# Performance work log

Measured on AMD Instinct MI355X. Metric: run time of the kernel, lower is better.

Reference implementation:

```python
import jax, jax.numpy as jnp
import numpy as np

MAX_BITS = 8   # codes are stored at 8 bits (max of supported_bits), 4 codes per int32
W_BITS = 4     # active bit-width -> lut has 2**W_BITS entries per output row


def setup_inputs() -> dict:
    key = jax.random.key(0)
    k1, k2, k3 = jax.random.split(key, 3)
    B, S = 1, 2048
    OUT, IN = 8192, 8192
    x = jax.random.normal(k1, (B, S, IN), dtype=jnp.float32)
    qweight = jax.random.randint(k2, (OUT, IN // 4), 0, 2147483647, dtype=jnp.int32)
    # per-output-channel lookup table for w_bits=4 -> 16 entries
    lut = jax.random.normal(k3, (OUT, 2 ** W_BITS), dtype=jnp.float32)
    return {"x": x, "qweight": qweight, "lut": lut}


def dequant_kbit(qweight, lut, w_bits):
    # qweight: (O, K//4) int32 -> 8-bit codes (O, K)
    O = qweight.shape[0]
    shifts = jnp.array([0, 8, 16, 24], dtype=jnp.int32)
    codes = (qweight[:, :, None] >> shifts) & 0xFF          # (O, K//4, 4)
    codes = codes.reshape(O, -1)                             # (O, K)
    # any-precision: top w_bits of the 8-bit code index the w_bits LUT
    idx = codes >> (MAX_BITS - w_bits)                       # (O, K) in [0, 2**w_bits)
    weight = jnp.take_along_axis(lut, idx, axis=1)           # (O, K)
    return weight


def reference(x, qweight, lut):
    # bulk path of AnyprecisionLinear.forward (tokens > 8): dequant then matmul
    weight = dequant_kbit(qweight, lut, W_BITS)              # (O, K)
    out = jnp.einsum('bsk,ok->bso', x, weight)               # (B, S, O)
    return out
```

## Files before the change

kernel.cpp:

```cpp
#include <hip/hip_runtime.h>
#include <stdint.h>


#define M_DIM 2048
#define N_DIM 8192
#define K_DIM 8192
#define BM 128
#define BN 128
#define BK 64

typedef __bf16 bf16x8 __attribute__((ext_vector_type(8)));
typedef float f32x16 __attribute__((ext_vector_type(16)));

__device__ __forceinline__ unsigned int f2bf(float f) {
  unsigned int u = __float_as_uint(f);
  return (u + 0x7FFFu + ((u >> 16) & 1u)) >> 16;
}

__global__ __launch_bounds__(256) void dequant_kernel(
    const int4* __restrict__ qw4,
    const float* __restrict__ lut,
    unsigned short* __restrict__ wb) {
  __shared__ unsigned int slut[4 * 16 * 64];
  const int wave = threadIdx.x >> 6;
  const int lane = threadIdx.x & 63;
  const int row = (blockIdx.x << 2) + wave;

  unsigned int* tbl = slut + wave * (16 * 64) + lane;
  const float* lr = lut + row * 16;
#pragma unroll
  for (int e = 0; e < 16; ++e) tbl[e * 64] = f2bf(lr[e]);

  const int4* src = qw4 + (size_t)row * 512 + lane;
  unsigned short* dst = wb + (size_t)row * K_DIM + lane * 16;

#pragma unroll
  for (int it = 0; it < 8; ++it) {
    int4 q = src[it * 64];
    unsigned int w[4] = {(unsigned int)q.x, (unsigned int)q.y,
                         (unsigned int)q.z, (unsigned int)q.w};
    unsigned int v[16];
#pragma unroll
    for (int j = 0; j < 4; ++j) {
#pragma unroll
      for (int k = 0; k < 4; ++k)
        v[j * 4 + k] = tbl[((w[j] >> (8 * k + 4)) & 15u) * 64];
    }
    uint4 o0, o1;
    o0.x = v[0] | (v[1] << 16);   o0.y = v[2]  | (v[3] << 16);
    o0.z = v[4] | (v[5] << 16);   o0.w = v[6]  | (v[7] << 16);
    o1.x = v[8] | (v[9] << 16);   o1.y = v[10] | (v[11] << 16);
    o1.z = v[12] | (v[13] << 16); o1.w = v[14] | (v[15] << 16);
    uint4* dp = (uint4*)(dst + it * 1024);
    dp[0] = o0;
    dp[1] = o1;
  }
}

__global__ __launch_bounds__(256) void cvt_x_kernel(
    const float4* __restrict__ x4, unsigned int* __restrict__ xb) {
  const int idx = blockIdx.x * 256 + threadIdx.x;
  float4 a = x4[2 * idx];
  float4 b = x4[2 * idx + 1];
  uint4 o;
  o.x = f2bf(a.x) | (f2bf(a.y) << 16);
  o.y = f2bf(a.z) | (f2bf(a.w) << 16);
  o.z = f2bf(b.x) | (f2bf(b.y) << 16);
  o.w = f2bf(b.z) | (f2bf(b.w) << 16);
  ((uint4*)xb)[idx] = o;
}

__global__ __launch_bounds__(256) void gemm_bt(
    const unsigned short* __restrict__ A,
    const unsigned short* __restrict__ B,
    float* __restrict__ C) {
  __shared__ __align__(16) unsigned short sA[BM * BK];
  __shared__ __align__(16) unsigned short sB[BN * BK];

  const int tid = threadIdx.x;
  const int wave = tid >> 6;
  const int lane = tid & 63;
  const int m0 = blockIdx.y * BM;
  const int n0 = blockIdx.x * BN;
  const int wm = (wave & 1) * 64;
  const int wn = (wave >> 1) * 64;

  const int srow = lane >> 3;
  const int scol = ((lane & 7) ^ (lane >> 3)) * 8;

  const int laneN = lane & 31;
  const int half = lane >> 5;
  const int sw = laneN & 7;

  f32x16 acc[2][2];
#pragma unroll
  for (int i = 0; i < 2; ++i)
#pragma unroll
    for (int j = 0; j < 2; ++j)
#pragma unroll
      for (int r = 0; r < 16; ++r) acc[i][j][r] = 0.0f;

  for (int k0 = 0; k0 < K_DIM; k0 += BK) {
#pragma unroll
    for (int r = 0; r < 4; ++r) {
      const int chunk = wave * 4 + r;
      const int row = chunk * 8 + srow;
      const unsigned short* ga = A + (size_t)(m0 + row) * K_DIM + k0 + scol;
      __builtin_amdgcn_global_load_lds(
          (const __attribute__((address_space(1))) void*)ga,
          (__attribute__((address_space(3))) void*)(sA + chunk * 512),
          16, 0, 0);
      const unsigned short* gb = B + (size_t)(n0 + row) * K_DIM + k0 + scol;
      __builtin_amdgcn_global_load_lds(
          (const __attribute__((address_space(1))) void*)gb,
          (__attribute__((address_space(3))) void*)(sB + chunk * 512),
          16, 0, 0);
    }
    __syncthreads();

#pragma unroll
    for (int kk = 0; kk < BK; kk += 16) {
      const int c = ((kk >> 3) + half) ^ sw;
      bf16x8 af[2], bfr[2];
#pragma unroll
      for (int t = 0; t < 2; ++t) {
        af[t]  = *(const bf16x8*)(sA + (wm + t * 32 + laneN) * BK + c * 8);
        bfr[t] = *(const bf16x8*)(sB + (wn + t * 32 + laneN) * BK + c * 8);
      }
#pragma unroll
      for (int i = 0; i < 2; ++i)
#pragma unroll
        for (int j = 0; j < 2; ++j)
          acc[i][j] = __builtin_amdgcn_mfma_f32_32x32x16_bf16(
              af[i], bfr[j], acc[i][j], 0, 0, 0);
    }
    __syncthreads();
  }

#pragma unroll
  for (int i = 0; i < 2; ++i)
#pragma unroll
    for (int j = 0; j < 2; ++j) {
      const int rbase = m0 + wm + i * 32 + 4 * half;
      const int col = n0 + wn + j * 32 + laneN;
#pragma unroll
      for (int r = 0; r < 16; ++r) {
        const int rrow = rbase + (r & 3) + 8 * (r >> 2);
        C[(size_t)rrow * N_DIM + col] = acc[i][j][r];
      }
    }
}

__global__ void naive_kernel(const float* __restrict__ x,
                             const int* __restrict__ qw,
                             const float* __restrict__ lut,
                             float* __restrict__ out) {
  int o = blockIdx.x * blockDim.x + threadIdx.x;
  int s = blockIdx.y;
  const float* xr = x + (size_t)s * K_DIM;
  const unsigned int* qr = (const unsigned int*)qw + (size_t)o * (K_DIM / 4);
  const float* l = lut + o * 16;
  float acc = 0.f;
  for (int w = 0; w < K_DIM / 4; ++w) {
    unsigned int q = qr[w];
    acc += xr[w * 4 + 0] * l[(q >> 4) & 15u]
         + xr[w * 4 + 1] * l[(q >> 12) & 15u]
         + xr[w * 4 + 2] * l[(q >> 20) & 15u]
         + xr[w * 4 + 3] * l[(q >> 28) & 15u];
  }
  out[(size_t)s * N_DIM + o] = acc;
}

extern "C" void kernel_launch(void* const* d_in, const int* in_sizes, int n_in,
                              void* d_out, int out_size, void* d_ws, size_t ws_size,
                              hipStream_t stream) {
  const float* x   = (const float*)d_in[0];
  const int*   qw  = (const int*)d_in[1];
  const float* lut = (const float*)d_in[2];
  float* out = (float*)d_out;

  const size_t wb_elems = (size_t)N_DIM * K_DIM;
  const size_t xb_elems = (size_t)M_DIM * K_DIM;
  const size_t need = (wb_elems + xb_elems) * sizeof(unsigned short);

  if (ws_size >= need) {
    unsigned short* wb = (unsigned short*)d_ws;
    unsigned short* xb = wb + wb_elems;

    hipLaunchKernelGGL(dequant_kernel, dim3(N_DIM / 4), dim3(256), 0, stream,
                       (const int4*)qw, lut, wb);

    const int n_thr = M_DIM * K_DIM / 8;
    hipLaunchKernelGGL(cvt_x_kernel, dim3(n_thr / 256), dim3(256), 0, stream,
                       (const float4*)x, (unsigned int*)xb);

    dim3 grid(N_DIM / BN, M_DIM / BM);
    hipLaunchKernelGGL(gemm_bt, grid, dim3(256), 0, stream, xb, wb, out);
  } else {
    dim3 grid(N_DIM / 256, M_DIM);
    hipLaunchKernelGGL(naive_kernel, grid, dim3(256), 0, stream, x, qw, lut, out);
  }
}
```

Measured before the change: 501.3 us.

## Rewrite GEMM as 256x256 tile with double-buffered LDS and interleaved prefetch

```diff
diff --git a/kernel.cpp b/kernel.cpp
--- a/kernel.cpp
+++ b/kernel.cpp
@@ -5,12 +5,13 @@
 #define M_DIM 2048
 #define N_DIM 8192
 #define K_DIM 8192
-#define BM 128
-#define BN 128
+#define BM 256
+#define BN 256
 #define BK 64
+#define KT (K_DIM / BK)
 
 typedef __bf16 bf16x8 __attribute__((ext_vector_type(8)));
-typedef float f32x16 __attribute__((ext_vector_type(16)));
+typedef float f32x4 __attribute__((ext_vector_type(4)));
 
 __device__ __forceinline__ unsigned int f2bf(float f) {
   unsigned int u = __float_as_uint(f);
@@ -70,85 +71,177 @@
   ((uint4*)xb)[idx] = o;
 }
 
-__global__ __launch_bounds__(256) void gemm_bt(
+
+__device__ __forceinline__ void stage_q(const unsigned short* __restrict__ g,
+                                        unsigned short* lds_tile, int grow0,
+                                        int qrow, int koff, int wave, int srow,
+                                        int scol) {
+  const unsigned short* src =
+      g + (size_t)(grow0 + qrow + (wave << 3) + srow) * K_DIM + koff + scol;
+  __builtin_amdgcn_global_load_lds(
+      (const __attribute__((address_space(1))) void*)src,
+      (__attribute__((address_space(3))) void*)(lds_tile +
+                                                (qrow + (wave << 3)) * BK),
+      16, 0, 0);
+}
+
+__device__ __forceinline__ void load_a4(const unsigned short* __restrict__ s,
+                                        int row0, int rrow, int rk,
+                                        bf16x8 out[4][2]) {
+#pragma unroll
+  for (int mi = 0; mi < 4; ++mi) {
+    const int row = row0 + mi * 16 + rrow;
+    const int sw = row & 7;
+#pragma unroll
+    for (int ks = 0; ks < 2; ++ks) {
+      const int slot = (ks * 4 + rk) ^ sw;
+      out[mi][ks] = *(const bf16x8*)(s + row * BK + slot * 8);
+    }
+  }
+}
+
+__device__ __forceinline__ void load_b2(const unsigned short* __restrict__ s,
+                                        int row0, int rrow, int rk,
+                                        bf16x8 out[2][2]) {
+#pragma unroll
+  for (int nj = 0; nj < 2; ++nj) {
+    const int row = row0 + nj * 16 + rrow;
+    const int sw = row & 7;
+#pragma unroll
+    for (int ks = 0; ks < 2; ++ks) {
+      const int slot = (ks * 4 + rk) ^ sw;
+      out[nj][ks] = *(const bf16x8*)(s + row * BK + slot * 8);
+    }
+  }
+}
+
+#define MFMA_Q(AH, BH)                                                        \
+  _Pragma("unroll")                                                           \
+  for (int ks = 0; ks < 2; ++ks)                                              \
+    _Pragma("unroll")                                                         \
+    for (int mi = 0; mi < 4; ++mi)                                            \
+      _Pragma("unroll")                                                       \
+      for (int nj = 0; nj < 2; ++nj)                                          \
+        acc[(AH)*4 + mi][(BH)*2 + nj] =                                       \
+            __builtin_amdgcn_mfma_f32_16x16x32_bf16(                          \
+                af[mi][ks], bq[nj][ks], acc[(AH)*4 + mi][(BH)*2 + nj], 0, 0, 0);
+
+#define SBAR asm volatile("s_barrier" ::: "memory")
+
+#define KTILE(T, BF)                                                          \
+  {                                                                           \
+    const int ko1 = (((T) + 1) & (KT - 1)) * BK;                              \
+    const int ko2 = (((T) + 2) & (KT - 1)) * BK;                              \
+    const unsigned short* sa_ = sA[BF];                                       \
+    const unsigned short* sb_ = sB[BF];                                       \
+    unsigned short* naA = sA[(BF) ^ 1];                                       \
+    unsigned short* naB = sB[(BF) ^ 1];                                       \
+    unsigned short* caA = sA[BF];                                             \
+                                                          \
+    load_a4(sa_, wm + 0, rrow, rk, af);                                       \
+    load_b2(sb_, wn + 0, rrow, rk, bq);                                       \
+    stage_q(A, naA, m0, 64, ko1, wave, srow, scol);                           \
+    stage_q(B, naB, n0, 0, ko1, wave, srow, scol);                            \
+    SBAR;                                                                     \
+    __builtin_amdgcn_s_setprio(1);                                            \
+    MFMA_Q(0, 0);                                                             \
+    __builtin_amdgcn_s_setprio(0);                                            \
+    SBAR;                                                                     \
+                                               \
+    load_b2(sb_, wn + 32, rrow, rk, bq);                                      \
+    stage_q(A, naA, m0, 192, ko1, wave, srow, scol);                          \
+    stage_q(B, naB, n0, 64, ko1, wave, srow, scol);                           \
+    SBAR;                                                                     \
+    __builtin_amdgcn_s_setprio(1);                                            \
+    MFMA_Q(0, 1);                                                             \
+    __builtin_amdgcn_s_setprio(0);                                            \
+    SBAR;                                                                     \
+                                               \
+    load_a4(sa_, wm + 64, rrow, rk, af);                                      \
+    stage_q(B, naB, n0, 128, ko1, wave, srow, scol);                          \
+    stage_q(B, naB, n0, 192, ko1, wave, srow, scol);                          \
+    SBAR;                                                                     \
+    __builtin_amdgcn_s_setprio(1);                                            \
+    MFMA_Q(1, 1);                                                             \
+    __builtin_amdgcn_s_setprio(0);                                            \
+    SBAR;                                                                     \
+                                               \
+    load_b2(sb_, wn + 0, rrow, rk, bq);                                       \
+    stage_q(A, caA, m0, 0, ko2, wave, srow, scol);                            \
+    stage_q(A, caA, m0, 128, ko2, wave, srow, scol);                          \
+    SBAR;                                                                     \
+    __builtin_amdgcn_s_setprio(1);                                            \
+    MFMA_Q(1, 0);                                                             \
+    __builtin_amdgcn_s_setprio(0);                                            \
+    asm volatile("s_waitcnt vmcnt(2)" ::: "memory");                          \
+    SBAR;                                                                     \
+  }
+
+__global__ __launch_bounds__(512, 2) void gemm_bt(
     const unsigned short* __restrict__ A,
     const unsigned short* __restrict__ B,
     float* __restrict__ C) {
-  __shared__ __align__(16) unsigned short sA[BM * BK];
-  __shared__ __align__(16) unsigned short sB[BN * BK];
+  __shared__ __align__(16) unsigned short sA[2][BM * BK];
+  __shared__ __align__(16) unsigned short sB[2][BN * BK];
 
   const int tid = threadIdx.x;
   const int wave = tid >> 6;
   const int lane = tid & 63;
-  const int m0 = blockIdx.y * BM;
-  const int n0 = blockIdx.x * BN;
-  const int wm = (wave & 1) * 64;
-  const int wn = (wave >> 1) * 64;
+
+  const int bid = blockIdx.x;
+  const int swz = (bid & 7) * 32 + (bid >> 3);
+  const int m0 = (swz >> 5) * BM;
+  const int n0 = (swz & 31) * BN;
+
+  const int wm = (wave >> 2) * 128;
+  const int wn = (wave & 3) * 64;
 
   const int srow = lane >> 3;
-  const int scol = ((lane & 7) ^ (lane >> 3)) * 8;
-
-  const int laneN = lane & 31;
-  const int half = lane >> 5;
-  const int sw = laneN & 7;
-
-  f32x16 acc[2][2];
-#pragma unroll
-  for (int i = 0; i < 2; ++i)
-#pragma unroll
-    for (int j = 0; j < 2; ++j)
-#pragma unroll
-      for (int r = 0; r < 16; ++r) acc[i][j][r] = 0.0f;
-
-  for (int k0 = 0; k0 < K_DIM; k0 += BK) {
-#pragma unroll
-    for (int r = 0; r < 4; ++r) {
-      const int chunk = wave * 4 + r;
-      const int row = chunk * 8 + srow;
-      const unsigned short* ga = A + (size_t)(m0 + row) * K_DIM + k0 + scol;
-      __builtin_amdgcn_global_load_lds(
-          (const __attribute__((address_space(1))) void*)ga,
-          (__attribute__((address_space(3))) void*)(sA + chunk * 512),
-          16, 0, 0);
-      const unsigned short* gb = B + (size_t)(n0 + row) * K_DIM + k0 + scol;
-      __builtin_amdgcn_global_load_lds(
-          (const __attribute__((address_space(1))) void*)gb,
-          (__attribute__((address_space(3))) void*)(sB + chunk * 512),
-          16, 0, 0);
-    }
-    __syncthreads();
-
-#pragma unroll
-    for (int kk = 0; kk < BK; kk += 16) {
-      const int c = ((kk >> 3) + half) ^ sw;
-      bf16x8 af[2], bfr[2];
-#pragma unroll
-      for (int t = 0; t < 2; ++t) {
-        af[t]  = *(const bf16x8*)(sA + (wm + t * 32 + laneN) * BK + c * 8);
-        bfr[t] = *(const bf16x8*)(sB + (wn + t * 32 + laneN) * BK + c * 8);
-      }
-#pragma unroll
-      for (int i = 0; i < 2; ++i)
-#pragma unroll
-        for (int j = 0; j < 2; ++j)
-          acc[i][j] = __builtin_amdgcn_mfma_f32_32x32x16_bf16(
-              af[i], bfr[j], acc[i][j], 0, 0, 0);
-    }
-    __syncthreads();
-  }
-
-#pragma unroll
-  for (int i = 0; i < 2; ++i)
-#pragma unroll
-    for (int j = 0; j < 2; ++j) {
-      const int rbase = m0 + wm + i * 32 + 4 * half;
-      const int col = n0 + wn + j * 32 + laneN;
-#pragma unroll
-      for (int r = 0; r < 16; ++r) {
-        const int rrow = rbase + (r & 3) + 8 * (r >> 2);
-        C[(size_t)rrow * N_DIM + col] = acc[i][j][r];
-      }
-    }
+  const int scol = ((lane & 7) ^ srow) * 8;
+
+  const int rrow = lane & 15;
+  const int rk = lane >> 4;
+
+  bf16x8 af[4][2];
+  bf16x8 bq[2][2];
+  f32x4 acc[8][4];
+#pragma unroll
+  for (int m = 0; m < 8; ++m)
+#pragma unroll
+    for (int n = 0; n < 4; ++n)
+#pragma unroll
+      for (int r = 0; r < 4; ++r) acc[m][n][r] = 0.0f;
+
+  stage_q(A, sA[0], m0, 0, 0, wave, srow, scol);
+  stage_q(A, sA[0], m0, 64, 0, wave, srow, scol);
+  stage_q(A, sA[0], m0, 128, 0, wave, srow, scol);
+  stage_q(A, sA[0], m0, 192, 0, wave, srow, scol);
+  stage_q(B, sB[0], n0, 0, 0, wave, srow, scol);
+  stage_q(B, sB[0], n0, 64, 0, wave, srow, scol);
+  stage_q(B, sB[0], n0, 128, 0, wave, srow, scol);
+  stage_q(B, sB[0], n0, 192, 0, wave, srow, scol);
+  stage_q(A, sA[1], m0, 0, BK, wave, srow, scol);
+  stage_q(A, sA[1], m0, 128, BK, wave, srow, scol);
+  asm volatile("s_waitcnt vmcnt(2)" ::: "memory");
+  SBAR;
+
+#pragma unroll 1
+  for (int tt = 0; tt < KT / 2; ++tt) {
+    KTILE(2 * tt, 0)
+    KTILE(2 * tt + 1, 1)
+  }
+  asm volatile("s_waitcnt vmcnt(0)" ::: "memory");
+
+  const int crow0 = m0 + wm + 4 * rk;
+  const int ccol0 = n0 + wn + rrow;
+#pragma unroll
+  for (int m = 0; m < 8; ++m)
+#pragma unroll
+    for (int n = 0; n < 4; ++n)
+#pragma unroll
+      for (int r = 0; r < 4; ++r)
+        C[(size_t)(crow0 + m * 16 + r) * N_DIM + ccol0 + n * 16] =
+            acc[m][n][r];
 }
 
 __global__ void naive_kernel(const float* __restrict__ x,
@@ -172,10 +265,10 @@
 }
 
 extern "C" void kernel_launch(void* const* d_in, const int* in_sizes, int n_in,
-                              void* d_out, int out_size, void* d_ws, size_t ws_size,
-                              hipStream_t stream) {
-  const float* x   = (const float*)d_in[0];
-  const int*   qw  = (const int*)d_in[1];
+                              void* d_out, int out_size, void* d_ws,
+                              size_t ws_size, hipStream_t stream) {
+  const float* x = (const float*)d_in[0];
+  const int* qw = (const int*)d_in[1];
   const float* lut = (const float*)d_in[2];
   float* out = (float*)d_out;
 
@@ -194,10 +287,11 @@
     hipLaunchKernelGGL(cvt_x_kernel, dim3(n_thr / 256), dim3(256), 0, stream,
                        (const float4*)x, (unsigned int*)xb);
 
-    dim3 grid(N_DIM / BN, M_DIM / BM);
-    hipLaunchKernelGGL(gemm_bt, grid, dim3(256), 0, stream, xb, wb, out);
+    hipLaunchKernelGGL(gemm_bt, dim3((M_DIM / BM) * (N_DIM / BN)), dim3(512),
+                       0, stream, xb, wb, out);
   } else {
     dim3 grid(N_DIM / 256, M_DIM);
-    hipLaunchKernelGGL(naive_kernel, grid, dim3(256), 0, stream, x, qw, lut, out);
-  }
-}
+    hipLaunchKernelGGL(naive_kernel, grid, dim3(256), 0, stream, x, qw, lut,
+                       out);
+  }
+}
```

Result: faster. 473.4 us (-5.6%).
